# Optimization experiments

Measured on AMD Instinct MI355X. Metric: run time of the kernel, lower is better.

## Reference

```python
import jax, jax.numpy as jnp
import numpy as np

DIM = 768
NUM_HEADS = 12
N_DIV = 8
T_SHIFT = 20
T_SPAN = 11
T_CUT = T_SHIFT + 1 - T_SPAN  # 10
C = DIM // NUM_HEADS          # 64 channels per head
FOLD = C // N_DIV             # 8
BATCH = 2
FRAMES = 32
K_WIN = 4
N_TOK = 196
B_TOT = BATCH * FRAMES * K_WIN  # 256


def _entmax15_last(x):
    """Exact entmax-1.5 (Peters & Martins) along the last axis."""
    x = (x - jnp.max(x, axis=-1, keepdims=True)) * 0.5
    xs = jnp.flip(jnp.sort(x, axis=-1), axis=-1)  # descending
    d = x.shape[-1]
    rho = jnp.arange(1, d + 1, dtype=x.dtype)
    mean = jnp.cumsum(xs, axis=-1) / rho
    meansq = jnp.cumsum(xs * xs, axis=-1) / rho
    ss = rho * (meansq - mean * mean)
    delta = (1.0 - ss) / rho
    pos = delta > 0
    sq = jnp.where(pos, jnp.sqrt(jnp.where(pos, delta, 1.0)), 0.0)
    tau = mean - sq
    support = jnp.sum(tau <= xs, axis=-1, keepdims=True)
    tau_star = jnp.take_along_axis(tau, support - 1, axis=-1)
    y = jnp.clip(x - tau_star, 0.0, None)
    return y * y


def entmax15(x, axis):
    return jnp.moveaxis(_entmax15_last(jnp.moveaxis(x, axis, -1)), -1, axis)


def _shift(feat, pool_w, pool_b, win_w, win_b, forward):
    # feat: [b, t, k, h, n, c]
    b, t, k, h, n, c = feat.shape
    f = N_DIV
    cp = c // f
    # 'b t k h n (c f) -> (k n h c) (b f) t'
    g = feat.reshape(b, t, k, h, n, cp, f)
    g = jnp.transpose(g, (2, 4, 3, 5, 0, 6, 1)).reshape(k * n * h * cp, b * f, t)
    pad = (T_SHIFT, 0) if forward else (0, T_SHIFT)
    g = jnp.pad(g, ((0, 0), (0, 0), pad))
    # 'b t k h n c -> b (k n t) (h c)'
    xk = jnp.transpose(feat, (0, 2, 4, 1, 3, 5)).reshape(b, k * n * t, h * c)
    attn = xk @ pool_w + pool_b                      # [b, knt, 1]
    pooled = jnp.sum(entmax15(attn, axis=1) * xk, axis=1)  # [b, dim]
    # 'b 1 (T f) -> (b f) 1 T'
    win = (pooled @ win_w + win_b).reshape(b, T_SPAN, f)
    win = jnp.transpose(win, (0, 2, 1)).reshape(b * f, 1, T_SPAN)
    win = _entmax15_last(win)
    # depthwise conv over the (b f) channel dim, batch dim = k*n*h*cp
    out = jax.lax.conv_general_dilated(
        g, win, (1,), 'VALID',
        dimension_numbers=('NCH', 'OIH', 'NCH'),
        feature_group_count=b * f)
    tp = t + T_CUT
    # '(k n h c) (b f) t -> b t k h n c f' then mean over f
    out = out.reshape(k, n, h, cp, b, f, tp)
    out = jnp.transpose(out, (4, 6, 0, 2, 1, 3, 5)).mean(axis=-1)  # [b, tp, k, h, n, cp]
    return out[:, :-T_CUT] if forward else out[:, T_CUT:]


def _pcs(x, batch_size, frame_len, fpw, fpb, bpw, bpb, fww, fwb, bww, bwb):
    B, h, n, c = x.shape
    k = B // (batch_size * frame_len)
    feat = x.reshape(batch_size, frame_len, k, h, n, c)
    fwd = _shift(feat, fpw, fpb, fww, fwb, True)
    bwd = _shift(feat, bpw, bpb, bww, bwb, False)
    out = jnp.concatenate([fwd, bwd, feat[..., 2 * FOLD:]], axis=-1)
    return out.reshape(B, h, n, c)


def setup_inputs() -> dict:
    key = jax.random.key(0)
    ks = jax.random.split(key, 6)
    s = 0.02
    return {
        'x': jax.random.normal(ks[0], (B_TOT, NUM_HEADS, N_TOK, C), dtype=jnp.float32),
        'batch_size': BATCH,
        'frame_len': FRAMES,
        'fwd_pool_w': jax.random.normal(ks[1], (DIM, 1), dtype=jnp.float32) * s,
        'fwd_pool_b': jnp.zeros((1,), dtype=jnp.float32),
        'bwd_pool_w': jax.random.normal(ks[2], (DIM, 1), dtype=jnp.float32) * s,
        'bwd_pool_b': jnp.zeros((1,), dtype=jnp.float32),
        'fwd_win_w': jax.random.normal(ks[3], (DIM, T_SPAN * N_DIV), dtype=jnp.float32) * s,
        'fwd_win_b': jnp.zeros((T_SPAN * N_DIV,), dtype=jnp.float32),
        'bwd_win_w': jax.random.normal(ks[4], (DIM, T_SPAN * N_DIV), dtype=jnp.float32) * s,
        'bwd_win_b': jnp.zeros((T_SPAN * N_DIV,), dtype=jnp.float32),
    }


def reference(x, batch_size, frame_len, fwd_pool_w, fwd_pool_b, bwd_pool_w, bwd_pool_b,
              fwd_win_w, fwd_win_b, bwd_win_w, bwd_win_b):
    return _pcs(x, batch_size, frame_len, fwd_pool_w, fwd_pool_b, bwd_pool_w, bwd_pool_b,
                fwd_win_w, fwd_win_b, bwd_win_w, bwd_win_b)
```

## Files before the change

kernel.cpp:

```cpp
#include <hip/hip_runtime.h>

#define NH 12
#define NTOK 196
#define TT 32
#define KW 4
#define NI 25088
#define TSTRIDE 602112

__global__ __launch_bounds__(256) void k_attn(
    const float4* __restrict__ x4, const float4* __restrict__ wf4,
    const float4* __restrict__ wb4, float* __restrict__ attn)
{
  __shared__ float4 swf[192], swb[192];
  int tid = threadIdx.x;
  if (tid < 192) { swf[tid] = wf4[tid]; swb[tid] = wb4[tid]; }
  __syncthreads();

  int B = blockIdx.y;
  int lane = tid & 63;
  int n = blockIdx.x * 16 + (tid >> 6) * 4 + (lane >> 4);
  int c4 = lane & 15;
  bool nv = (n < NTOK);
  float accf = 0.f, accb = 0.f;
  #pragma unroll
  for (int h = 0; h < NH; h++) {
    float4 xv = make_float4(0.f, 0.f, 0.f, 0.f);
    if (nv) xv = x4[((B * NH + h) * NTOK + n) * 16 + c4];
    float4 wf = swf[h * 16 + c4];
    float4 wb = swb[h * 16 + c4];
    accf += xv.x * wf.x + xv.y * wf.y + xv.z * wf.z + xv.w * wf.w;
    accb += xv.x * wb.x + xv.y * wb.y + xv.z * wb.z + xv.w * wb.w;
  }
  #pragma unroll
  for (int m = 1; m < 16; m <<= 1) {
    accf += __shfl_xor(accf, m);
    accb += __shfl_xor(accb, m);
  }
  if (nv && (lane & 15) == 0) {
    int b = B >> 7, t = (B >> 2) & 31, k = B & 3;
    int i = (k * NTOK + n) * TT + t;
    attn[(0 * 2 + b) * NI + i] = accf;
    attn[(1 * 2 + b) * NI + i] = accb;
  }
}

__global__ __launch_bounds__(1024) void k_entmax_pool(
    const float* __restrict__ attn, const float* __restrict__ x,
    float* __restrict__ pooled)
{
  int p = blockIdx.x;
  int b = p & 1;
  const float* a = attn + p * NI;
  int tid = threadIdx.x;
  float v[25];
  float mx = -3.0e38f;
  #pragma unroll
  for (int r = 0; r < 25; r++) {
    int i = r * 1024 + tid;
    v[r] = (i < NI) ? a[i] : -3.0e38f;
    mx = fmaxf(mx, v[r]);
  }
  __shared__ float sred1[16];
  __shared__ float sred2[16];
  __shared__ float sbc;
  int wv = tid >> 6;
  #pragma unroll
  for (int m = 1; m < 64; m <<= 1) mx = fmaxf(mx, __shfl_xor(mx, m));
  if ((tid & 63) == 0) sred1[wv] = mx;
  __syncthreads();
  if (tid == 0) {
    float m2 = sred1[0];
    for (int i2 = 1; i2 < 16; i2++) m2 = fmaxf(m2, sred1[i2]);
    sbc = m2;
  }
  __syncthreads();
  float amax = sbc;
  #pragma unroll
  for (int r = 0; r < 25; r++) v[r] = 0.5f * (v[r] - amax);
  float tau = -1.0f;
  for (int it = 0; it < 8; it++) {
    float s2 = 0.f, s1 = 0.f;
    #pragma unroll
    for (int r = 0; r < 25; r++) {
      float d = fmaxf(v[r] - tau, 0.f);
      s2 += d * d;
      s1 += d;
    }
    #pragma unroll
    for (int m = 1; m < 64; m <<= 1) {
      s2 += __shfl_xor(s2, m);
      s1 += __shfl_xor(s1, m);
    }
    if ((tid & 63) == 0) { sred2[wv] = s2; sred1[wv] = s1; }
    __syncthreads();
    if (tid == 0) {
      float S2 = 0.f, S1 = 0.f;
      for (int i2 = 0; i2 < 16; i2++) { S2 += sred2[i2]; S1 += sred1[i2]; }
      sbc = tau + (S2 - 1.f) / fmaxf(2.f * S1, 1e-12f);
    }
    __syncthreads();
    tau = sbc;
    __syncthreads();
  }
  __shared__ int scnt;
  __shared__ int sidx[8192];
  __shared__ float swgt[8192];
  if (tid == 0) scnt = 0;
  __syncthreads();
  #pragma unroll
  for (int r = 0; r < 25; r++) {
    float d = v[r] - tau;
    if (d > 0.f) {
      int slot = atomicAdd(&scnt, 1);
      if (slot < 8192) { sidx[slot] = r * 1024 + tid; swgt[slot] = d * d; }
    }
  }
  __syncthreads();
  int count = min(scnt, 8192);
  if (tid < 768) {
    int h = tid >> 6, c = tid & 63;
    float acc = 0.f;
    for (int e = 0; e < count; e++) {
      int i = sidx[e];
      float w = swgt[e];
      int t = i & 31, r2 = i >> 5;
      int n = r2 % NTOK, k = r2 / NTOK;
      int B = (b * TT + t) * KW + k;
      acc += w * x[((B * NH + h) * NTOK + n) * 64 + c];
    }
    pooled[p * 768 + tid] = acc;
  }
}

__global__ __launch_bounds__(704) void k_win(
    const float* __restrict__ pooled,
    const float* __restrict__ fww, const float* __restrict__ fwb,
    const float* __restrict__ bww, const float* __restrict__ bwb,
    float* __restrict__ winout)
{
  int p = blockIdx.x;
  const float* ww = (p >> 1) ? bww : fww;
  const float* wb = (p >> 1) ? bwb : fwb;
  const float* pl = pooled + p * 768;
  int tid = threadIdx.x;
  int rseg = tid / 88, col = tid % 88;
  __shared__ float part[8][88];
  __shared__ float praw[88];
  float acc = 0.f;
  #pragma unroll 8
  for (int j = 0; j < 96; j++) {
    int r = rseg * 96 + j;
    acc += pl[r] * ww[r * 88 + col];
  }
  part[rseg][col] = acc;
  __syncthreads();
  if (tid < 88) {
    float s = wb[tid];
    #pragma unroll
    for (int g = 0; g < 8; g++) s += part[g][tid];
    praw[tid] = s;
  }
  __syncthreads();
  if (tid < 8) {
    int f = tid;
    float v[11];
    float mx = -3.0e38f;
    #pragma unroll
    for (int j = 0; j < 11; j++) { v[j] = praw[j * 8 + f]; mx = fmaxf(mx, v[j]); }
    #pragma unroll
    for (int j = 0; j < 11; j++) v[j] = 0.5f * (v[j] - mx);
    float lo = -1.f, hi = 0.f;
    for (int it = 0; it < 30; it++) {
      float mid = 0.5f * (lo + hi);
      float s = 0.f;
      #pragma unroll
      for (int j = 0; j < 11; j++) { float d = fmaxf(v[j] - mid, 0.f); s += d * d; }
      if (s >= 1.f) lo = mid; else hi = mid;
    }
    float tau = 0.5f * (lo + hi);
    #pragma unroll
    for (int j = 0; j < 11; j++) {
      float d = fmaxf(v[j] - tau, 0.f);
      winout[p * 88 + f * 11 + j] = d * d * 0.125f;
    }
  }
}

__global__ __launch_bounds__(256) void k_shift(
    const float* __restrict__ x, const float* __restrict__ win,
    float* __restrict__ out)
{
  int bkh = blockIdx.y;
  int b = bkh / 48, rem = bkh % 48;
  int k = rem / 12, h = rem % 12;
  int wave = threadIdx.x >> 6, lane = threadIdx.x & 63;
  int n = blockIdx.x * 4 + wave;
  int f = lane & 7;
  float wjf[11], wjb[11];
  #pragma unroll
  for (int j = 0; j < 11; j++) {
    wjf[j] = win[(0 * 2 + b) * 88 + f * 11 + j];
    wjb[j] = win[(1 * 2 + b) * 88 + f * 11 + j];
  }
  int base = ((b * 128 + k) * NH + h) * 12544 + n * 64 + lane;
  float xr[32];
  #pragma unroll
  for (int tp = 0; tp < 32; tp++) xr[tp] = x[base + tp * TSTRIDE];

  float accF[32];
  #pragma unroll
  for (int t = 0; t < 32; t++) accF[t] = 0.f;
  #pragma unroll
  for (int tp = 0; tp <= 21; tp++) {
    #pragma unroll
    for (int j = 0; j < 11; j++) {
      int to = tp + 20 - j;
      if (to >= 0 && to < 32) accF[to] += wjf[j] * xr[tp];
    }
  }
  #pragma unroll
  for (int t = 0; t < 32; t++) {
    float s = accF[t];
    s += __shfl_xor(s, 1);
    s += __shfl_xor(s, 2);
    s += __shfl_xor(s, 4);
    accF[t] = s;
  }

  float accB[32];
  #pragma unroll
  for (int t = 0; t < 32; t++) accB[t] = 0.f;
  #pragma unroll
  for (int tp = 10; tp < 32; tp++) {
    #pragma unroll
    for (int j = 0; j < 11; j++) {
      int to = tp - 10 - j;
      if (to >= 0 && to < 32) accB[to] += wjb[j] * xr[tp];
    }
  }
  #pragma unroll
  for (int t = 0; t < 32; t++) {
    float s = accB[t];
    s += __shfl_xor(s, 1);
    s += __shfl_xor(s, 2);
    s += __shfl_xor(s, 4);
    accB[t] = s;
  }

  int src = (lane & 7) << 3;
  #pragma unroll
  for (int t = 0; t < 32; t++) {
    float sf = __shfl(accF[t], src);
    float sb = __shfl(accB[t], src);
    float val = (lane < 8) ? sf : (lane < 16) ? sb : xr[t];
    __builtin_nontemporal_store(val, &out[base + t * TSTRIDE]);
  }
}

extern "C" void kernel_launch(void* const* d_in, const int* in_sizes, int n_in,
                              void* d_out, int out_size, void* d_ws, size_t ws_size,
                              hipStream_t stream)
{
  (void)in_sizes; (void)n_in; (void)out_size; (void)ws_size;
  const float* x   = (const float*)d_in[0];
  const float* fpw = (const float*)d_in[3];
  const float* bpw = (const float*)d_in[5];
  const float* fww = (const float*)d_in[7];
  const float* fwb = (const float*)d_in[8];
  const float* bww = (const float*)d_in[9];
  const float* bwb = (const float*)d_in[10];
  float* out = (float*)d_out;

  float* W      = (float*)d_ws;
  float* attn   = W;
  float* pooled = attn + 4 * NI;
  float* winb   = pooled + 3072;

  dim3 g1(13, 256);
  k_attn<<<g1, 256, 0, stream>>>((const float4*)x, (const float4*)fpw,
                                 (const float4*)bpw, attn);
  k_entmax_pool<<<4, 1024, 0, stream>>>(attn, x, pooled);
  k_win<<<4, 704, 0, stream>>>(pooled, fww, fwb, bww, bwb, winb);
  dim3 g5(49, 96);
  k_shift<<<g5, 256, 0, stream>>>(x, winb, out);
}
```

Baseline: 339.3 us.

## Fuse all four stages into one persistent kernel with global atomic barriers

Replaces the four kernel launches with a single persistent kernel of 512 blocks. Blocks first compute attention logits in grid-stride fashion. The last four blocks to arrive at a ticket counter then do the entmax pooling and the window projection, while the other blocks prefetch the window weights. All blocks then spin on a global flag before running the shift convolution. This removes launch gaps and per-kernel tail effects, at the cost of spin-waiting, larger register arrays (98 per thread) and the risk of deadlock if not all blocks are co-resident.

```diff
diff --git a/kernel.cpp b/kernel.cpp
--- a/kernel.cpp
+++ b/kernel.cpp
@@ -6,254 +6,305 @@
 #define KW 4
 #define NI 25088
 #define TSTRIDE 602112
-
-__global__ __launch_bounds__(256) void k_attn(
-    const float4* __restrict__ x4, const float4* __restrict__ wf4,
-    const float4* __restrict__ wb4, float* __restrict__ attn)
+#define NBLK 512
+#define NWAVES (NBLK * 4)
+
+__device__ int g_counter1;
+__device__ int g_flag1;
+__device__ int g_counter2;
+__device__ int g_flag2;
+
+__global__ __launch_bounds__(256, 2) void k_fused(
+    const float* __restrict__ x, const float4* __restrict__ wf4,
+    const float4* __restrict__ wb4,
+    const float* __restrict__ fww, const float* __restrict__ fwb,
+    const float* __restrict__ bww, const float* __restrict__ bwb,
+    float* __restrict__ attn, float* __restrict__ winb,
+    float* __restrict__ out)
 {
   __shared__ float4 swf[192], swb[192];
+  __shared__ int   sidx[4096];
+  __shared__ float swgt[4096];
+  __shared__ float spool4[4][768];
+  __shared__ float spool[768];
+  __shared__ float part[2][88];
+  __shared__ float praw[88];
+  __shared__ float sred1[4], sred2[4];
+  __shared__ float sbc;
+  __shared__ int   scnt, sticket, ssetter;
+
   int tid = threadIdx.x;
+  int wave = tid >> 6, lane = tid & 63;
   if (tid < 192) { swf[tid] = wf4[tid]; swb[tid] = wb4[tid]; }
   __syncthreads();
 
-  int B = blockIdx.y;
-  int lane = tid & 63;
-  int n = blockIdx.x * 16 + (tid >> 6) * 4 + (lane >> 4);
-  int c4 = lane & 15;
-  bool nv = (n < NTOK);
-  float accf = 0.f, accb = 0.f;
-  #pragma unroll
-  for (int h = 0; h < NH; h++) {
-    float4 xv = make_float4(0.f, 0.f, 0.f, 0.f);
-    if (nv) xv = x4[((B * NH + h) * NTOK + n) * 16 + c4];
-    float4 wf = swf[h * 16 + c4];
-    float4 wb = swb[h * 16 + c4];
-    accf += xv.x * wf.x + xv.y * wf.y + xv.z * wf.z + xv.w * wf.w;
-    accb += xv.x * wb.x + xv.y * wb.y + xv.z * wb.z + xv.w * wb.w;
-  }
-  #pragma unroll
-  for (int m = 1; m < 16; m <<= 1) {
-    accf += __shfl_xor(accf, m);
-    accb += __shfl_xor(accb, m);
-  }
-  if (nv && (lane & 15) == 0) {
-    int b = B >> 7, t = (B >> 2) & 31, k = B & 3;
-    int i = (k * NTOK + n) * TT + t;
-    attn[(0 * 2 + b) * NI + i] = accf;
-    attn[(1 * 2 + b) * NI + i] = accb;
-  }
-}
-
-__global__ __launch_bounds__(1024) void k_entmax_pool(
-    const float* __restrict__ attn, const float* __restrict__ x,
-    float* __restrict__ pooled)
-{
-  int p = blockIdx.x;
-  int b = p & 1;
-  const float* a = attn + p * NI;
-  int tid = threadIdx.x;
-  float v[25];
-  float mx = -3.0e38f;
-  #pragma unroll
-  for (int r = 0; r < 25; r++) {
-    int i = r * 1024 + tid;
-    v[r] = (i < NI) ? a[i] : -3.0e38f;
-    mx = fmaxf(mx, v[r]);
-  }
-  __shared__ float sred1[16];
-  __shared__ float sred2[16];
-  __shared__ float sbc;
-  int wv = tid >> 6;
-  #pragma unroll
-  for (int m = 1; m < 64; m <<= 1) mx = fmaxf(mx, __shfl_xor(mx, m));
-  if ((tid & 63) == 0) sred1[wv] = mx;
-  __syncthreads();
-  if (tid == 0) {
-    float m2 = sred1[0];
-    for (int i2 = 1; i2 < 16; i2++) m2 = fmaxf(m2, sred1[i2]);
-    sbc = m2;
+  const float4* x4 = (const float4*)x;
+  int gw = blockIdx.x * 4 + wave;
+  int c4 = lane & 15, nq = lane >> 4;
+  for (int tsk = gw; tsk < 256 * 49; tsk += NWAVES) {
+    int B = tsk / 49, ngrp = tsk % 49;
+    int n = ngrp * 4 + nq;
+    float accf = 0.f, accb = 0.f;
+    #pragma unroll
+    for (int h = 0; h < NH; h++) {
+      float4 xv = x4[((B * NH + h) * NTOK + n) * 16 + c4];
+      float4 wf = swf[h * 16 + c4], wb = swb[h * 16 + c4];
+      accf += xv.x * wf.x + xv.y * wf.y + xv.z * wf.z + xv.w * wf.w;
+      accb += xv.x * wb.x + xv.y * wb.y + xv.z * wb.z + xv.w * wb.w;
+    }
+    #pragma unroll
+    for (int m = 1; m < 16; m <<= 1) {
+      accf += __shfl_xor(accf, m);
+      accb += __shfl_xor(accb, m);
+    }
+    if ((lane & 15) == 0) {
+      int b = B >> 7, t = (B >> 2) & 31, k = B & 3;
+      int i = (k * NTOK + n) * TT + t;
+      attn[b * NI + i] = accf;
+      attn[(2 + b) * NI + i] = accb;
+    }
   }
   __syncthreads();
-  float amax = sbc;
-  #pragma unroll
-  for (int r = 0; r < 25; r++) v[r] = 0.5f * (v[r] - amax);
-  float tau = -1.0f;
-  for (int it = 0; it < 8; it++) {
-    float s2 = 0.f, s1 = 0.f;
-    #pragma unroll
-    for (int r = 0; r < 25; r++) {
-      float d = fmaxf(v[r] - tau, 0.f);
-      s2 += d * d;
-      s1 += d;
-    }
-    #pragma unroll
-    for (int m = 1; m < 64; m <<= 1) {
-      s2 += __shfl_xor(s2, m);
-      s1 += __shfl_xor(s1, m);
-    }
-    if ((tid & 63) == 0) { sred2[wv] = s2; sred1[wv] = s1; }
-    __syncthreads();
-    if (tid == 0) {
-      float S2 = 0.f, S1 = 0.f;
-      for (int i2 = 0; i2 < 16; i2++) { S2 += sred2[i2]; S1 += sred1[i2]; }
-      sbc = tau + (S2 - 1.f) / fmaxf(2.f * S1, 1e-12f);
-    }
-    __syncthreads();
-    tau = sbc;
-    __syncthreads();
-  }
-  __shared__ int scnt;
-  __shared__ int sidx[8192];
-  __shared__ float swgt[8192];
-  if (tid == 0) scnt = 0;
+  if (tid == 0)
+    sticket = __hip_atomic_fetch_add(&g_counter1, 1, __ATOMIC_ACQ_REL,
+                                     __HIP_MEMORY_SCOPE_AGENT);
   __syncthreads();
-  #pragma unroll
-  for (int r = 0; r < 25; r++) {
-    float d = v[r] - tau;
-    if (d > 0.f) {
-      int slot = atomicAdd(&scnt, 1);
-      if (slot < 8192) { sidx[slot] = r * 1024 + tid; swgt[slot] = d * d; }
-    }
-  }
-  __syncthreads();
-  int count = min(scnt, 8192);
-  if (tid < 768) {
-    int h = tid >> 6, c = tid & 63;
-    float acc = 0.f;
-    for (int e = 0; e < count; e++) {
+  int ticket = sticket;
+  int iter = ticket / NBLK, rank = ticket % NBLK;
+  int target = iter + 1;
+
+  if (rank == NBLK - 1 && tid == 0)
+    __hip_atomic_store(&g_flag1, target, __ATOMIC_RELEASE,
+                       __HIP_MEMORY_SCOPE_AGENT);
+
+  bool need_spin2 = true;
+
+  if (rank >= NBLK - 4) {
+    if (rank != NBLK - 1) {
+      int spins = 0;
+      while (__hip_atomic_load(&g_flag1, __ATOMIC_RELAXED,
+                               __HIP_MEMORY_SCOPE_AGENT) < target) {
+        __builtin_amdgcn_s_sleep(2);
+        if (++spins > (1 << 20)) break;
+      }
+      (void)__hip_atomic_load(&g_flag1, __ATOMIC_ACQUIRE,
+                              __HIP_MEMORY_SCOPE_AGENT);
+    }
+    int p = rank - (NBLK - 4);
+    int b = p & 1;
+    const float* a = attn + p * NI;
+
+    float v[98];
+    float mx = -3.0e38f;
+    #pragma unroll
+    for (int r = 0; r < 98; r++) {
+      v[r] = a[r * 256 + tid];
+      mx = fmaxf(mx, v[r]);
+    }
+    #pragma unroll
+    for (int m = 1; m < 64; m <<= 1) mx = fmaxf(mx, __shfl_xor(mx, m));
+    if (lane == 0) sred1[wave] = mx;
+    __syncthreads();
+    if (tid == 0)
+      sbc = fmaxf(fmaxf(sred1[0], sred1[1]), fmaxf(sred1[2], sred1[3]));
+    __syncthreads();
+    float amax = sbc;
+    #pragma unroll
+    for (int r = 0; r < 98; r++) v[r] = 0.5f * (v[r] - amax);
+
+    float tau = -1.0f;
+    for (int it = 0; it < 8; it++) {
+      float s2 = 0.f, s1 = 0.f;
+      #pragma unroll
+      for (int r = 0; r < 98; r++) {
+        float d = fmaxf(v[r] - tau, 0.f);
+        s2 += d * d;
+        s1 += d;
+      }
+      #pragma unroll
+      for (int m = 1; m < 64; m <<= 1) {
+        s2 += __shfl_xor(s2, m);
+        s1 += __shfl_xor(s1, m);
+      }
+      if (lane == 0) { sred2[wave] = s2; sred1[wave] = s1; }
+      __syncthreads();
+      if (tid == 0) {
+        float S2 = sred2[0] + sred2[1] + sred2[2] + sred2[3];
+        float S1 = sred1[0] + sred1[1] + sred1[2] + sred1[3];
+        sbc = tau + (S2 - 1.f) / fmaxf(2.f * S1, 1e-12f);
+      }
+      __syncthreads();
+      tau = sbc;
+      __syncthreads();
+    }
+
+    if (tid == 0) scnt = 0;
+    __syncthreads();
+    #pragma unroll
+    for (int r = 0; r < 98; r++) {
+      float d = v[r] - tau;
+      if (d > 0.f) {
+        int slot = atomicAdd(&scnt, 1);
+        if (slot < 4096) { sidx[slot] = r * 256 + tid; swgt[slot] = d * d; }
+      }
+    }
+    __syncthreads();
+    int count = min(scnt, 4096);
+
+    float acc12[12];
+    #pragma unroll
+    for (int h = 0; h < 12; h++) acc12[h] = 0.f;
+    for (int e = wave; e < count; e += 4) {
       int i = sidx[e];
       float w = swgt[e];
       int t = i & 31, r2 = i >> 5;
       int n = r2 % NTOK, k = r2 / NTOK;
       int B = (b * TT + t) * KW + k;
-      acc += w * x[((B * NH + h) * NTOK + n) * 64 + c];
-    }
-    pooled[p * 768 + tid] = acc;
+      const float* xb = x + (size_t)B * (NH * NTOK * 64) + n * 64 + lane;
+      #pragma unroll
+      for (int h = 0; h < 12; h++) acc12[h] += w * xb[h * (NTOK * 64)];
+    }
+    #pragma unroll
+    for (int h = 0; h < 12; h++) spool4[wave][h * 64 + lane] = acc12[h];
+    __syncthreads();
+    #pragma unroll
+    for (int q = 0; q < 3; q++) {
+      int j = q * 256 + tid;
+      spool[j] = spool4[0][j] + spool4[1][j] + spool4[2][j] + spool4[3][j];
+    }
+    __syncthreads();
+
+    if (tid < 176) {
+      int rseg = tid / 88, col = tid % 88;
+      const float* ww = (p >> 1) ? bww : fww;
+      float accw = 0.f;
+      #pragma unroll 8
+      for (int j = 0; j < 384; j++) {
+        int r = rseg * 384 + j;
+        accw += spool[r] * ww[r * 88 + col];
+      }
+      part[rseg][col] = accw;
+    }
+    __syncthreads();
+    if (tid < 88) {
+      const float* wbv = (p >> 1) ? bwb : fwb;
+      praw[tid] = wbv[tid] + part[0][tid] + part[1][tid];
+    }
+    __syncthreads();
+    if (tid < 8) {
+      int f = tid;
+      float vv[11];
+      float mmx = -3.0e38f;
+      #pragma unroll
+      for (int j = 0; j < 11; j++) { vv[j] = praw[j * 8 + f]; mmx = fmaxf(mmx, vv[j]); }
+      #pragma unroll
+      for (int j = 0; j < 11; j++) vv[j] = 0.5f * (vv[j] - mmx);
+      float lo = -1.f, hi = 0.f;
+      for (int it = 0; it < 30; it++) {
+        float mid = 0.5f * (lo + hi), s = 0.f;
+        #pragma unroll
+        for (int j = 0; j < 11; j++) { float d = fmaxf(vv[j] - mid, 0.f); s += d * d; }
+        if (s >= 1.f) lo = mid; else hi = mid;
+      }
+      float tw = 0.5f * (lo + hi);
+      #pragma unroll
+      for (int j = 0; j < 11; j++) {
+        float d = fmaxf(vv[j] - tw, 0.f);
+        winb[p * 88 + f * 11 + j] = d * d * 0.125f;
+      }
+    }
+    __syncthreads();
+    if (tid == 0) {
+      int t2 = __hip_atomic_fetch_add(&g_counter2, 1, __ATOMIC_ACQ_REL,
+                                      __HIP_MEMORY_SCOPE_AGENT);
+      if ((t2 & 3) == 3) {
+        __hip_atomic_store(&g_flag2, target, __ATOMIC_RELEASE,
+                           __HIP_MEMORY_SCOPE_AGENT);
+        ssetter = 1;
+      } else ssetter = 0;
+    }
+    __syncthreads();
+    need_spin2 = (ssetter == 0);
+  } else {
+    int idx = rank * 256 + tid;
+    if (idx < 768 * 88 / 4) {
+      float4 t1 = ((const float4*)fww)[idx];
+      float4 t2 = ((const float4*)bww)[idx];
+      asm volatile("" :: "v"(t1.x), "v"(t2.x));
+    }
   }
-}
-
-__global__ __launch_bounds__(704) void k_win(
-    const float* __restrict__ pooled,
-    const float* __restrict__ fww, const float* __restrict__ fwb,
-    const float* __restrict__ bww, const float* __restrict__ bwb,
-    float* __restrict__ winout)
-{
-  int p = blockIdx.x;
-  const float* ww = (p >> 1) ? bww : fww;
-  const float* wb = (p >> 1) ? bwb : fwb;
-  const float* pl = pooled + p * 768;
-  int tid = threadIdx.x;
-  int rseg = tid / 88, col = tid % 88;
-  __shared__ float part[8][88];
-  __shared__ float praw[88];
-  float acc = 0.f;
-  #pragma unroll 8
-  for (int j = 0; j < 96; j++) {
-    int r = rseg * 96 + j;
-    acc += pl[r] * ww[r * 88 + col];
+
+  if (need_spin2) {
+    int spins = 0;
+    while (__hip_atomic_load(&g_flag2, __ATOMIC_RELAXED,
+                             __HIP_MEMORY_SCOPE_AGENT) < target) {
+      __builtin_amdgcn_s_sleep(32);
+      if (++spins > (1 << 20)) break;
+    }
+    (void)__hip_atomic_load(&g_flag2, __ATOMIC_ACQUIRE,
+                            __HIP_MEMORY_SCOPE_AGENT);
   }
-  part[rseg][col] = acc;
-  __syncthreads();
-  if (tid < 88) {
-    float s = wb[tid];
-    #pragma unroll
-    for (int g = 0; g < 8; g++) s += part[g][tid];
-    praw[tid] = s;
-  }
-  __syncthreads();
-  if (tid < 8) {
-    int f = tid;
-    float v[11];
-    float mx = -3.0e38f;
-    #pragma unroll
-    for (int j = 0; j < 11; j++) { v[j] = praw[j * 8 + f]; mx = fmaxf(mx, v[j]); }
-    #pragma unroll
-    for (int j = 0; j < 11; j++) v[j] = 0.5f * (v[j] - mx);
-    float lo = -1.f, hi = 0.f;
-    for (int it = 0; it < 30; it++) {
-      float mid = 0.5f * (lo + hi);
-      float s = 0.f;
-      #pragma unroll
-      for (int j = 0; j < 11; j++) { float d = fmaxf(v[j] - mid, 0.f); s += d * d; }
-      if (s >= 1.f) lo = mid; else hi = mid;
-    }
-    float tau = 0.5f * (lo + hi);
+
+  for (int tsk = gw; tsk < 96 * NTOK; tsk += NWAVES) {
+    int bkh = tsk / NTOK, n = tsk % NTOK;
+    int b = bkh / 48, rem = bkh % 48;
+    int k = rem / 12, h = rem % 12;
+    int f = lane & 7;
+    float wjf[11], wjb[11];
     #pragma unroll
     for (int j = 0; j < 11; j++) {
-      float d = fmaxf(v[j] - tau, 0.f);
-      winout[p * 88 + f * 11 + j] = d * d * 0.125f;
-    }
-  }
-}
-
-__global__ __launch_bounds__(256) void k_shift(
-    const float* __restrict__ x, const float* __restrict__ win,
-    float* __restrict__ out)
-{
-  int bkh = blockIdx.y;
-  int b = bkh / 48, rem = bkh % 48;
-  int k = rem / 12, h = rem % 12;
-  int wave = threadIdx.x >> 6, lane = threadIdx.x & 63;
-  int n = blockIdx.x * 4 + wave;
-  int f = lane & 7;
-  float wjf[11], wjb[11];
-  #pragma unroll
-  for (int j = 0; j < 11; j++) {
-    wjf[j] = win[(0 * 2 + b) * 88 + f * 11 + j];
-    wjb[j] = win[(1 * 2 + b) * 88 + f * 11 + j];
-  }
-  int base = ((b * 128 + k) * NH + h) * 12544 + n * 64 + lane;
-  float xr[32];
-  #pragma unroll
-  for (int tp = 0; tp < 32; tp++) xr[tp] = x[base + tp * TSTRIDE];
-
-  float accF[32];
-  #pragma unroll
-  for (int t = 0; t < 32; t++) accF[t] = 0.f;
-  #pragma unroll
-  for (int tp = 0; tp <= 21; tp++) {
-    #pragma unroll
-    for (int j = 0; j < 11; j++) {
-      int to = tp + 20 - j;
-      if (to >= 0 && to < 32) accF[to] += wjf[j] * xr[tp];
-    }
-  }
-  #pragma unroll
-  for (int t = 0; t < 32; t++) {
-    float s = accF[t];
-    s += __shfl_xor(s, 1);
-    s += __shfl_xor(s, 2);
-    s += __shfl_xor(s, 4);
-    accF[t] = s;
-  }
-
-  float accB[32];
-  #pragma unroll
-  for (int t = 0; t < 32; t++) accB[t] = 0.f;
-  #pragma unroll
-  for (int tp = 10; tp < 32; tp++) {
-    #pragma unroll
-    for (int j = 0; j < 11; j++) {
-      int to = tp - 10 - j;
-      if (to >= 0 && to < 32) accB[to] += wjb[j] * xr[tp];
-    }
-  }
-  #pragma unroll
-  for (int t = 0; t < 32; t++) {
-    float s = accB[t];
-    s += __shfl_xor(s, 1);
-    s += __shfl_xor(s, 2);
-    s += __shfl_xor(s, 4);
-    accB[t] = s;
-  }
-
-  int src = (lane & 7) << 3;
-  #pragma unroll
-  for (int t = 0; t < 32; t++) {
-    float sf = __shfl(accF[t], src);
-    float sb = __shfl(accB[t], src);
-    float val = (lane < 8) ? sf : (lane < 16) ? sb : xr[t];
-    __builtin_nontemporal_store(val, &out[base + t * TSTRIDE]);
+      wjf[j] = winb[b * 88 + f * 11 + j];
+      wjb[j] = winb[(2 + b) * 88 + f * 11 + j];
+    }
+    int base = ((b * 128 + k) * NH + h) * 12544 + n * 64 + lane;
+    float xr[32];
+    #pragma unroll
+    for (int tp = 0; tp < 32; tp++) xr[tp] = x[base + tp * TSTRIDE];
+
+    int src = (lane & 7) << 3;
+    float val[32];
+    float acc[32];
+
+    #pragma unroll
+    for (int t = 0; t < 32; t++) acc[t] = 0.f;
+    #pragma unroll
+    for (int tp = 0; tp <= 21; tp++) {
+      #pragma unroll
+      for (int j = 0; j < 11; j++) {
+        int to = tp + 20 - j;
+        if (to >= 0 && to < 32) acc[to] += wjf[j] * xr[tp];
+      }
+    }
+    #pragma unroll
+    for (int t = 0; t < 32; t++) {
+      float s = acc[t];
+      s += __shfl_xor(s, 1);
+      s += __shfl_xor(s, 2);
+      s += __shfl_xor(s, 4);
+      float sf = __shfl(s, src);
+      val[t] = (lane < 8) ? sf : xr[t];
+    }
+
+    #pragma unroll
+    for (int t = 0; t < 32; t++) acc[t] = 0.f;
+    #pragma unroll
+    for (int tp = 10; tp < 32; tp++) {
+      #pragma unroll
+      for (int j = 0; j < 11; j++) {
+        int to = tp - 10 - j;
+        if (to >= 0 && to < 32) acc[to] += wjb[j] * xr[tp];
+      }
+    }
+    #pragma unroll
+    for (int t = 0; t < 32; t++) {
+      float s = acc[t];
+      s += __shfl_xor(s, 1);
+      s += __shfl_xor(s, 2);
+      s += __shfl_xor(s, 4);
+      float sb = __shfl(s, src);
+      if (lane >= 8 && lane < 16) val[t] = sb;
+      __builtin_nontemporal_store(val[t], &out[base + t * TSTRIDE]);
+    }
   }
 }
 
@@ -271,16 +322,10 @@
   const float* bwb = (const float*)d_in[10];
   float* out = (float*)d_out;
 
-  float* W      = (float*)d_ws;
-  float* attn   = W;
-  float* pooled = attn + 4 * NI;
-  float* winb   = pooled + 3072;
-
-  dim3 g1(13, 256);
-  k_attn<<<g1, 256, 0, stream>>>((const float4*)x, (const float4*)fpw,
-                                 (const float4*)bpw, attn);
-  k_entmax_pool<<<4, 1024, 0, stream>>>(attn, x, pooled);
-  k_win<<<4, 704, 0, stream>>>(pooled, fww, fwb, bww, bwb, winb);
-  dim3 g5(49, 96);
-  k_shift<<<g5, 256, 0, stream>>>(x, winb, out);
+  float* W    = (float*)d_ws;
+  float* attn = W;
+  float* winb = attn + 4 * NI;
+
+  k_fused<<<NBLK, 256, 0, stream>>>(x, (const float4*)fpw, (const float4*)bpw,
+                                    fww, fwb, bww, bwb, attn, winb, out);
 }
```

Measured after the change: 420.1 us. +23.8%, slower.
